# Kernel optimization log

Measured on AMD Instinct MI355X. Metric: run time of the kernel, lower is better.

## Reference

```python
import jax, jax.numpy as jnp
import numpy as np

H, NH, NKV, HD, FF = 2048, 16, 8, 128, 6144
S, T = 2048, 4096
EPS, THETA, NEG = 1e-6, 1e6, -1e9

def _rms(x, w, eps=EPS):
    return x * jax.lax.rsqrt(jnp.mean(x * x, axis=-1, keepdims=True) + eps) * w

def _rotate_half(x):
    d = x.shape[-1] // 2
    return jnp.concatenate([-x[..., d:], x[..., :d]], axis=-1)

def _rope(positions, hd, theta=THETA):
    inv_freq = 1.0 / (theta ** (jnp.arange(0, hd, 2, dtype=jnp.float32) / hd))
    freqs = positions.astype(jnp.float32)[..., None] * inv_freq  # [B,S,hd/2]
    emb = jnp.concatenate([freqs, freqs], axis=-1)               # [B,S,hd]
    return jnp.cos(emb), jnp.sin(emb)

def setup_inputs() -> dict:
    key = jax.random.key(0)
    ks = jax.random.split(key, 12)
    hidden_states = jax.random.normal(ks[0], (1, S, H), jnp.float32) * 0.02
    i = jnp.arange(T)
    causal_mask = jnp.where(i[None, :] <= i[:, None], 0.0, NEG).astype(jnp.float32)[None, None]
    idxs = jnp.sort(jax.random.randint(ks[1], (S,), 0, T - 1, jnp.int32)).at[-1].set(T - 1)
    w = lambda k, sh: jax.random.normal(k, sh, jnp.float32) * 0.02
    return dict(
        hidden_states=hidden_states, causal_mask=causal_mask,
        keys_idxs=idxs, hs_idxs=idxs, positions=idxs[None, :],
        ln_in_w=jnp.ones((H,), jnp.float32),
        q_w=w(ks[2], (H, NH * HD)), k_w=w(ks[3], (H, NKV * HD)), v_w=w(ks[4], (H, NKV * HD)),
        q_norm_w=jnp.ones((HD,), jnp.float32), k_norm_w=jnp.ones((HD,), jnp.float32),
        o_w=w(ks[5], (NH * HD, H)), ln_post_w=jnp.ones((H,), jnp.float32),
        gate_w=w(ks[6], (H, FF)), up_w=w(ks[7], (H, FF)), down_w=w(ks[8], (FF, H)),
    )

def reference(hidden_states, causal_mask, keys_idxs, hs_idxs, positions,
              ln_in_w, q_w, k_w, v_w, q_norm_w, k_norm_w, o_w,
              ln_post_w, gate_w, up_w, down_w):
    B, Sq, _ = hidden_states.shape
    hd = q_norm_w.shape[0]
    nh = q_w.shape[1] // hd
    nkv = k_w.shape[1] // hd
    scaling = hd ** -0.5

    # gather pruned causal mask: index_select dim 3 (keys), then dim 2 (queries)
    mask = causal_mask[:, :, :, keys_idxs][:, :, hs_idxs, :]  # [B,1,Sq,Sk]

    cos, sin = _rope(positions, hd)  # [B,Sq,hd]

    x = _rms(hidden_states, ln_in_w)
    q = _rms((x @ q_w).reshape(B, Sq, nh, hd), q_norm_w).swapaxes(1, 2)   # [B,nh,Sq,hd]
    k = _rms((x @ k_w).reshape(B, Sq, nkv, hd), k_norm_w).swapaxes(1, 2)  # [B,nkv,Sq,hd]
    v = (x @ v_w).reshape(B, Sq, nkv, hd).swapaxes(1, 2)

    c, s = cos[:, None], sin[:, None]
    q = q * c + _rotate_half(q) * s
    k = k * c + _rotate_half(k) * s

    groups = nh // nkv
    k_rep = jnp.repeat(k, groups, axis=1)
    v_rep = jnp.repeat(v, groups, axis=1)

    # token-importance from last query (last original token kept at slot Sq-1)
    q_last = q[:, :, -1:, :]
    imp = jax.nn.softmax(jnp.einsum('bhqd,bhkd->bhqk', q_last, k_rep) * scaling, axis=-1)
    importance = imp[0, :, 0, :].mean(axis=0)
    importance = jax.lax.stop_gradient(importance.at[Sq - 1].set(jnp.inf))

    scores = jnp.einsum('bhqd,bhkd->bhqk', q, k_rep) * scaling + mask
    attn = jax.nn.softmax(scores, axis=-1)
    ctx = jnp.einsum('bhqk,bhkd->bhqd', attn, v_rep)
    attn_out = ctx.swapaxes(1, 2).reshape(B, Sq, nh * hd) @ o_w

    h = hidden_states + attn_out
    y = _rms(h, ln_post_w)
    mlp = (jax.nn.silu(y @ gate_w) * (y @ up_w)) @ down_w
    out = h + mlp
    return out, importance
```

## Files before the change

kernel.cpp:

```cpp
#include <hip/hip_runtime.h>
#include <math.h>

#define S_LEN 2048
#define HDIM  2048
#define NHEADS 16
#define NKVH   8
#define HD     128
#define FFDIM  6144
#define EPSV   1e-6f

__device__ __forceinline__ ushort f2bf(float f) {
    unsigned u = __float_as_uint(f);
    u += 0x7FFF + ((u >> 16) & 1);
    return (ushort)(u >> 16);
}
__device__ __forceinline__ float bf2f(ushort h) {
    return __uint_as_float(((unsigned)h) << 16);
}

typedef __attribute__((ext_vector_type(8))) short bf16x8;
typedef __attribute__((ext_vector_type(4))) float f32x4;

__device__ __forceinline__ void glds16(const void* g, void* l) {
    __builtin_amdgcn_global_load_lds(
        (const __attribute__((address_space(1))) void*)g,
        (__attribute__((address_space(3))) void*)l, 16, 0, 0);
}

__global__ __launch_bounds__(256) void rmsnorm_split_k(const float* __restrict__ in,
                                                       const float* __restrict__ w,
                                                       ushort* __restrict__ oh,
                                                       ushort* __restrict__ ol) {
    int s = blockIdx.x;
    int tid = threadIdx.x;
    const float* row = in + (size_t)s * HDIM;
    float ss = 0.0f;
    for (int i = tid; i < HDIM; i += 256) {
        float v = row[i];
        ss += v * v;
    }
    __shared__ float red[256];
    red[tid] = ss;
    __syncthreads();
    for (int off = 128; off > 0; off >>= 1) {
        if (tid < off) red[tid] += red[tid + off];
        __syncthreads();
    }
    float r = rsqrtf(red[0] / (float)HDIM + EPSV);
    for (int i = tid; i < HDIM; i += 256) {
        float v = row[i] * r * w[i];
        ushort h = f2bf(v);
        oh[(size_t)s * HDIM + i] = h;
        ol[(size_t)s * HDIM + i] = f2bf(v - bf2f(h));
    }
}

__global__ __launch_bounds__(256) void split_k(const float* __restrict__ in,
                                               ushort* __restrict__ oh,
                                               ushort* __restrict__ ol, int n) {
    int i = blockIdx.x * 256 + threadIdx.x;
    if (i < n) {
        float v = in[i];
        ushort h = f2bf(v);
        oh[i] = h;
        ol[i] = f2bf(v - bf2f(h));
    }
}

__global__ __launch_bounds__(256) void conv_k_swz_k(const float* __restrict__ in,
                                                    ushort* __restrict__ oh,
                                                    ushort* __restrict__ ol) {
    int i = blockIdx.x * 256 + threadIdx.x;
    int s = i >> 10;
    int d = i & 127;
    int base = i & ~127;
    float v = in[i];
    unsigned u = __float_as_uint(v);
    float hi = __uint_as_float(u & 0xFFFF0000u);
    int o = base + (d ^ ((s & 7) << 3));
    oh[o] = (ushort)(u >> 16);
    ol[o] = (ushort)(__float_as_uint(v - hi) >> 16);
}

__global__ __launch_bounds__(256) void conv_vt_k(const float* __restrict__ v,
                                                 ushort* __restrict__ oh,
                                                 ushort* __restrict__ ol) {
    __shared__ float t[64][65];
    int s0 = blockIdx.x * 64, d0 = blockIdx.y * 64, kvh = blockIdx.z;
    int tid = threadIdx.x;
#pragma unroll
    for (int p = 0; p < 4; ++p) {
        int c = tid + p * 256;
        int ss = c >> 4, d4 = (c & 15) * 4;
        float4 x = *(const float4*)&v[((size_t)(s0 + ss) * NKVH + kvh) * HD + d0 + d4];
        t[d4 + 0][ss] = x.x;
        t[d4 + 1][ss] = x.y;
        t[d4 + 2][ss] = x.z;
        t[d4 + 3][ss] = x.w;
    }
    __syncthreads();
#pragma unroll
    for (int p = 0; p < 4; ++p) {
        int c = tid + p * 256;
        int dd = c >> 4, s4 = (c & 15) * 4;
        int d = d0 + dd;
        int sx = s4 ^ ((d & 7) << 3);
        size_t obase = ((size_t)kvh * HD + d) * S_LEN + s0 + sx;
        ushort4 hv, lv;
        float a0 = t[dd][s4 + 0], a1 = t[dd][s4 + 1], a2 = t[dd][s4 + 2], a3 = t[dd][s4 + 3];
        unsigned u0 = __float_as_uint(a0), u1 = __float_as_uint(a1);
        unsigned u2 = __float_as_uint(a2), u3 = __float_as_uint(a3);
        hv.x = (ushort)(u0 >> 16); lv.x = (ushort)(__float_as_uint(a0 - __uint_as_float(u0 & 0xFFFF0000u)) >> 16);
        hv.y = (ushort)(u1 >> 16); lv.y = (ushort)(__float_as_uint(a1 - __uint_as_float(u1 & 0xFFFF0000u)) >> 16);
        hv.z = (ushort)(u2 >> 16); lv.z = (ushort)(__float_as_uint(a2 - __uint_as_float(u2 & 0xFFFF0000u)) >> 16);
        hv.w = (ushort)(u3 >> 16); lv.w = (ushort)(__float_as_uint(a3 - __uint_as_float(u3 & 0xFFFF0000u)) >> 16);
        *(ushort4*)&oh[obase] = hv;
        *(ushort4*)&ol[obase] = lv;
    }
}

__global__ __launch_bounds__(256) void transpose_split_k(const float* __restrict__ W,
                                                         ushort* __restrict__ Th,
                                                         ushort* __restrict__ Tl,
                                                         int K, int Ntot, int n0) {
    __shared__ float t[64][65];
    int tid = threadIdx.x;
    int nt = blockIdx.x * 64;
    int kt = blockIdx.y * 64;
#pragma unroll
    for (int p = 0; p < 4; ++p) {
        int idx = tid + p * 256;
        int kk = idx >> 4;
        int nn = (idx & 15) * 4;
        float4 v = *(const float4*)&W[(size_t)(kt + kk) * Ntot + n0 + nt + nn];
        t[nn + 0][kk] = v.x;
        t[nn + 1][kk] = v.y;
        t[nn + 2][kk] = v.z;
        t[nn + 3][kk] = v.w;
    }
    __syncthreads();
#pragma unroll
    for (int p = 0; p < 4; ++p) {
        int idx = tid + p * 256;
        int nn = idx >> 4;
        int kk = (idx & 15) * 4;
        ushort4 hv, lv;
        float a0 = t[nn][kk + 0], a1 = t[nn][kk + 1], a2 = t[nn][kk + 2], a3 = t[nn][kk + 3];
        hv.x = f2bf(a0); lv.x = f2bf(a0 - bf2f(hv.x));
        hv.y = f2bf(a1); lv.y = f2bf(a1 - bf2f(hv.y));
        hv.z = f2bf(a2); lv.z = f2bf(a2 - bf2f(hv.z));
        hv.w = f2bf(a3); lv.w = f2bf(a3 - bf2f(hv.w));
        size_t o = (size_t)(nt + nn) * K + kt + kk;
        *(ushort4*)&Th[o] = hv;
        *(ushort4*)&Tl[o] = lv;
    }
}

template <int MODE>
__global__ __launch_bounds__(256, 3) void gemm_bf16x3(
    const ushort* __restrict__ Ah, const ushort* __restrict__ Al,
    const ushort* __restrict__ Bh, const ushort* __restrict__ Bl,
    const float* res, const float* __restrict__ gbuf,
    float* C, ushort* __restrict__ Dh, ushort* __restrict__ Dl,
    int M, int N, int K) {
    __shared__ __align__(16) ushort sA[2 * 64 * 32];
    __shared__ __align__(16) ushort sB[2 * 128 * 32];

    unsigned nbx = gridDim.x;
    unsigned flat = blockIdx.y * nbx + blockIdx.x;
    unsigned cpx = (nbx * gridDim.y) >> 3;
    unsigned sflat = (flat & 7u) * cpx + (flat >> 3);
    int bx = (int)(sflat % nbx);
    int by = (int)(sflat / nbx);
    int bm = by * 64, bn = bx * 128;

    int tid = threadIdx.x;
    int lane = tid & 63, wave = tid >> 6;

    int srow = tid >> 2;
    int sk = (tid & 3) * 8;
    const ushort* gAh = Ah + (size_t)(bm + srow) * K + sk;
    const ushort* gAl = Al + (size_t)(bm + srow) * K + sk;
    const ushort* gB0h = Bh + (size_t)(bn + srow) * K + sk;
    const ushort* gB0l = Bl + (size_t)(bn + srow) * K + sk;
    const ushort* gB1h = Bh + (size_t)(bn + 64 + srow) * K + sk;
    const ushort* gB1l = Bl + (size_t)(bn + 64 + srow) * K + sk;
    ushort* lAh = sA + tid * 8;
    ushort* lAl = sA + 2048 + tid * 8;
    ushort* lB0h = sB + tid * 8;
    ushort* lB1h = sB + 2048 + tid * 8;
    ushort* lB0l = sB + 4096 + tid * 8;
    ushort* lB1l = sB + 6144 + tid * 8;

    int r = lane & 15, kq = lane >> 4;
    const ushort* pA = sA + r * 32 + kq * 8;
    const ushort* pB = sB + (wave * 32 + r) * 32 + kq * 8;

    f32x4 acc[4][2] = {};

    for (int k0 = 0; k0 < K; k0 += 32) {
        glds16(gAh, lAh);
        glds16(gAl, lAl);
        glds16(gB0h, lB0h);
        glds16(gB1h, lB1h);
        glds16(gB0l, lB0l);
        glds16(gB1l, lB1l);
        gAh += 32; gAl += 32; gB0h += 32; gB0l += 32; gB1h += 32; gB1l += 32;
        __syncthreads();

        bf16x8 ah[4], al[4], bh[2], bl[2];
#pragma unroll
        for (int mi = 0; mi < 4; ++mi) {
            ah[mi] = *(const bf16x8*)(pA + mi * 512);
            al[mi] = *(const bf16x8*)(pA + 2048 + mi * 512);
        }
#pragma unroll
        for (int ni = 0; ni < 2; ++ni) {
            bh[ni] = *(const bf16x8*)(pB + ni * 512);
            bl[ni] = *(const bf16x8*)(pB + 4096 + ni * 512);
        }
#pragma unroll
        for (int mi = 0; mi < 4; ++mi)
#pragma unroll
            for (int ni = 0; ni < 2; ++ni) {
                acc[mi][ni] = __builtin_amdgcn_mfma_f32_16x16x32_bf16(ah[mi], bh[ni], acc[mi][ni], 0, 0, 0);
                acc[mi][ni] = __builtin_amdgcn_mfma_f32_16x16x32_bf16(al[mi], bh[ni], acc[mi][ni], 0, 0, 0);
                acc[mi][ni] = __builtin_amdgcn_mfma_f32_16x16x32_bf16(ah[mi], bl[ni], acc[mi][ni], 0, 0, 0);
            }
        __syncthreads();
    }

    int c0 = bn + wave * 32 + (lane & 15);
    int r0 = bm + (lane >> 4) * 4;
#pragma unroll
    for (int mi = 0; mi < 4; ++mi)
#pragma unroll
        for (int ni = 0; ni < 2; ++ni)
#pragma unroll
            for (int j = 0; j < 4; ++j) {
                int row = r0 + mi * 16 + j;
                int col = c0 + ni * 16;
                size_t idx = (size_t)row * N + col;
                float val = acc[mi][ni][j];
                if (MODE == 0) {
                    if (res) val += res[idx];
                    C[idx] = val;
                } else {
                    float gv = gbuf[idx];
                    float dv = gv / (1.0f + expf(-gv)) * val;
                    ushort hh = f2bf(dv);
                    Dh[idx] = hh;
                    Dl[idx] = f2bf(dv - bf2f(hh));
                }
            }
}

__global__ __launch_bounds__(128) void qk_norm_rope_k(float* __restrict__ qk,
                                                      const float* __restrict__ nw,
                                                      const int* __restrict__ positions,
                                                      int nheads) {
    int s = blockIdx.x;
    int h = blockIdx.y;
    int d = threadIdx.x;
    float* row = qk + ((size_t)s * nheads + h) * HD;
    __shared__ float buf[HD];
    __shared__ float red[HD];
    float v = row[d];
    red[d] = v * v;
    __syncthreads();
    for (int off = 64; off > 0; off >>= 1) {
        if (d < off) red[d] += red[d + off];
        __syncthreads();
    }
    float r = rsqrtf(red[0] / (float)HD + EPSV);
    float nv = v * r * nw[d];
    buf[d] = nv;
    __syncthreads();
    float pos = (float)positions[s];
    int d2 = d & 63;
    float inv_freq = expf(-((float)(2 * d2) / 128.0f) * 13.815510557964274f);
    float freq = pos * inv_freq;
    float c, sn;
    sincosf(freq, &sn, &c);
    float rot = (d < 64) ? -buf[d + 64] : buf[d - 64];
    row[d] = nv * c + rot * sn;
}

#define ATQ 64
#define ATK 64

__global__ __launch_bounds__(256, 2) void attn_mfma_k(
    const ushort* __restrict__ Qhg, const ushort* __restrict__ Qlg,
    const ushort* __restrict__ Khg, const ushort* __restrict__ Klg,
    const ushort* __restrict__ Vhg, const ushort* __restrict__ Vlg,
    const int* __restrict__ keys_idxs, const int* __restrict__ hs_idxs,
    float* __restrict__ ctx) {
    __shared__ __align__(16) ushort sKh[64 * 128];
    __shared__ __align__(16) ushort sKl[64 * 128];
    __shared__ __align__(16) ushort sVh[128 * 64];
    __shared__ __align__(16) ushort sVl[128 * 64];
    __shared__ int kidx[ATK];
    __shared__ int qpos[ATQ];

    int bx = blockIdx.x;
    int qt = (bx & 1) ? (31 - (bx >> 1)) : (bx >> 1);
    int h = blockIdx.y;
    int kvh = h >> 1;
    int tid = threadIdx.x;
    int lane = tid & 63, wv = tid >> 6;
    int q0 = qt * ATQ;
    int r = lane & 15, kq = lane >> 4;
    int xorv = (lane & 7) << 3;
    const float scale = 0.088388347648318447f;

    bf16x8 qh[4], ql[4];
    {
        const ushort* qb = Qhg + ((size_t)(q0 + wv * 16 + r) * NHEADS + h) * HD + kq * 8;
        const ushort* qb2 = Qlg + ((size_t)(q0 + wv * 16 + r) * NHEADS + h) * HD + kq * 8;
#pragma unroll
        for (int ks = 0; ks < 4; ++ks) {
            qh[ks] = *(const bf16x8*)(qb + ks * 32);
            ql[ks] = *(const bf16x8*)(qb2 + ks * 32);
        }
    }
    if (tid < ATQ) qpos[tid] = hs_idxs[q0 + tid];

    const size_t kvstride = (size_t)NKVH * HD;
    const ushort* gKh = Khg + ((size_t)(tid >> 4) * NKVH + kvh) * HD + (tid & 15) * 8;
    const ushort* gKl = Klg + ((size_t)(tid >> 4) * NKVH + kvh) * HD + (tid & 15) * 8;
    const ushort* gVh = Vhg + ((size_t)kvh * HD + (tid >> 3)) * S_LEN + (tid & 7) * 8;
    const ushort* gVl = Vlg + ((size_t)kvh * HD + (tid >> 3)) * S_LEN + (tid & 7) * 8;

    f32x4 o[8] = {};
    float m_run[4] = {-3.0e38f, -3.0e38f, -3.0e38f, -3.0e38f};
    float l_run[4] = {0.0f, 0.0f, 0.0f, 0.0f};

    __syncthreads();
    int hs_max = qpos[ATQ - 1];
    int qp[4];
#pragma unroll
    for (int j = 0; j < 4; ++j) qp[j] = qpos[wv * 16 + kq * 4 + j];

    for (int kt = 0; kt < S_LEN / ATK; ++kt) {
        int k0 = kt * ATK;
        if (keys_idxs[k0] > hs_max) break;
        __syncthreads();
        const size_t koff = (size_t)k0 * kvstride;
#pragma unroll
        for (int p = 0; p < 4; ++p) {
            glds16(gKh + koff + (size_t)p * 16 * kvstride, sKh + (tid + p * 256) * 8);
            glds16(gKl + koff + (size_t)p * 16 * kvstride, sKl + (tid + p * 256) * 8);
            glds16(gVh + k0 + (size_t)p * 32 * S_LEN, sVh + (tid + p * 256) * 8);
            glds16(gVl + k0 + (size_t)p * 32 * S_LEN, sVl + (tid + p * 256) * 8);
        }
        if (tid < ATK) kidx[tid] = keys_idxs[k0 + tid];
        __syncthreads();

        f32x4 sf[4] = {};
#pragma unroll
        for (int ks = 0; ks < 4; ++ks) {
            int kb = (ks * 32 + kq * 8) ^ xorv;
#pragma unroll
            for (int f = 0; f < 4; ++f) {
                bf16x8 kh = *(const bf16x8*)(sKh + (f * 16 + r) * 128 + kb);
                bf16x8 kl = *(const bf16x8*)(sKl + (f * 16 + r) * 128 + kb);
                sf[f] = __builtin_amdgcn_mfma_f32_16x16x32_bf16(qh[ks], kh, sf[f], 0, 0, 0);
                sf[f] = __builtin_amdgcn_mfma_f32_16x16x32_bf16(ql[ks], kh, sf[f], 0, 0, 0);
                sf[f] = __builtin_amdgcn_mfma_f32_16x16x32_bf16(qh[ks], kl, sf[f], 0, 0, 0);
            }
        }

        int kj[4];
#pragma unroll
        for (int f = 0; f < 4; ++f) kj[f] = kidx[f * 16 + r];
        float alj[4];
#pragma unroll
        for (int j = 0; j < 4; ++j) {
#pragma unroll
            for (int f = 0; f < 4; ++f)
                sf[f][j] = sf[f][j] * scale + ((kj[f] <= qp[j]) ? 0.0f : -1.0e9f);
            float m0 = fmaxf(fmaxf(sf[0][j], sf[1][j]), fmaxf(sf[2][j], sf[3][j]));
#pragma unroll
            for (int off = 1; off < 16; off <<= 1) m0 = fmaxf(m0, __shfl_xor(m0, off));
            float mn = fmaxf(m_run[j], m0);
            alj[j] = __expf(m_run[j] - mn);
            m_run[j] = mn;
            float rsum = 0.0f;
#pragma unroll
            for (int f = 0; f < 4; ++f) {
                sf[f][j] = __expf(sf[f][j] - mn);
                rsum += sf[f][j];
            }
#pragma unroll
            for (int off = 1; off < 16; off <<= 1) rsum += __shfl_xor(rsum, off);
            l_run[j] = l_run[j] * alj[j] + rsum;
        }
#pragma unroll
        for (int df = 0; df < 8; ++df)
#pragma unroll
            for (int j = 0; j < 4; ++j) o[df][j] *= alj[j];

        __syncthreads();

        ushort* sPh = sKh + wv * 2048;
        ushort* sPl = sPh + 1024;
#pragma unroll
        for (int j = 0; j < 4; ++j) {
            int qloc = kq * 4 + j;
            int swz = (qloc & 7) << 3;
            int rowb = qloc * 64;
#pragma unroll
            for (int f = 0; f < 4; ++f) {
                float pv = sf[f][j];
                unsigned u = __float_as_uint(pv);
                float hi = __uint_as_float(u & 0xFFFF0000u);
                int a = rowb + ((f * 16 + r) ^ swz);
                sPh[a] = (ushort)(u >> 16);
                sPl[a] = (ushort)(__float_as_uint(pv - hi) >> 16);
            }
        }

#pragma unroll
        for (int kv0 = 0; kv0 < 2; ++kv0) {
            int kb = (kv0 * 32 + kq * 8) ^ xorv;
            bf16x8 pah = *(const bf16x8*)(sPh + r * 64 + kb);
            bf16x8 pal = *(const bf16x8*)(sPl + r * 64 + kb);
#pragma unroll
            for (int df = 0; df < 8; ++df) {
                bf16x8 vh = *(const bf16x8*)(sVh + (df * 16 + r) * 64 + kb);
                bf16x8 vl = *(const bf16x8*)(sVl + (df * 16 + r) * 64 + kb);
                o[df] = __builtin_amdgcn_mfma_f32_16x16x32_bf16(pah, vh, o[df], 0, 0, 0);
                o[df] = __builtin_amdgcn_mfma_f32_16x16x32_bf16(pal, vh, o[df], 0, 0, 0);
                o[df] = __builtin_amdgcn_mfma_f32_16x16x32_bf16(pah, vl, o[df], 0, 0, 0);
            }
        }
    }

#pragma unroll
    for (int j = 0; j < 4; ++j) {
        float invl = 1.0f / l_run[j];
        int qg = q0 + wv * 16 + kq * 4 + j;
#pragma unroll
        for (int df = 0; df < 8; ++df) {
            int d = df * 16 + r;
            ctx[((size_t)qg * NHEADS + h) * HD + d] = o[df][j] * invl;
        }
    }
}

__global__ __launch_bounds__(256) void importance_scores_k(const float* __restrict__ q,
                                                           const float* __restrict__ k,
                                                           float* __restrict__ imp_ws) {
    int h = blockIdx.x;
    int kv = h >> 1;
    int tid = threadIdx.x;
    __shared__ float qrow[HD];
    __shared__ float sc[S_LEN];
    __shared__ float red[256];
    const float* qp = q + ((size_t)(S_LEN - 1) * NHEADS + h) * HD;
    if (tid < HD) qrow[tid] = qp[tid];
    __syncthreads();
    const float scale = 0.088388347648318447f;
    float lmax = -3.0e38f;
#pragma unroll
    for (int rep = 0; rep < 8; ++rep) {
        int j = tid + rep * 256;
        const float* kp = k + ((size_t)j * NKVH + kv) * HD;
        float dot = 0.0f;
        for (int d = 0; d < HD; ++d) dot += qrow[d] * kp[d];
        float sval = dot * scale;
        sc[j] = sval;
        lmax = fmaxf(lmax, sval);
    }
    red[tid] = lmax;
    __syncthreads();
    for (int off = 128; off > 0; off >>= 1) {
        if (tid < off) red[tid] = fmaxf(red[tid], red[tid + off]);
        __syncthreads();
    }
    float m = red[0];
    __syncthreads();
    float lsum = 0.0f;
    float evals[8];
#pragma unroll
    for (int rep = 0; rep < 8; ++rep) {
        int j = tid + rep * 256;
        float e = expf(sc[j] - m);
        evals[rep] = e;
        lsum += e;
    }
    red[tid] = lsum;
    __syncthreads();
    for (int off = 128; off > 0; off >>= 1) {
        if (tid < off) red[tid] += red[tid + off];
        __syncthreads();
    }
    float inv = 1.0f / red[0];
#pragma unroll
    for (int rep = 0; rep < 8; ++rep) {
        int j = tid + rep * 256;
        imp_ws[(size_t)h * S_LEN + j] = evals[rep] * inv;
    }
}

__global__ __launch_bounds__(256) void importance_combine_k(const float* __restrict__ imp_ws,
                                                            float* __restrict__ out) {
    int j = blockIdx.x * 256 + threadIdx.x;
    float sum = 0.0f;
    for (int h = 0; h < NHEADS; ++h) sum += imp_ws[(size_t)h * S_LEN + j];
    out[j] = (j == S_LEN - 1) ? 3.0e38f : sum * (1.0f / NHEADS);
}

extern "C" void kernel_launch(void* const* d_in, const int* in_sizes, int n_in,
                              void* d_out, int out_size, void* d_ws, size_t ws_size,
                              hipStream_t stream) {
    const float* hidden    = (const float*)d_in[0];
    const int*   keys_idxs = (const int*)d_in[2];
    const int*   hs_idxs   = (const int*)d_in[3];
    const int*   positions = (const int*)d_in[4];
    const float* ln_in_w   = (const float*)d_in[5];
    const float* q_w       = (const float*)d_in[6];
    const float* k_w       = (const float*)d_in[7];
    const float* v_w       = (const float*)d_in[8];
    const float* q_norm_w  = (const float*)d_in[9];
    const float* k_norm_w  = (const float*)d_in[10];
    const float* o_w       = (const float*)d_in[11];
    const float* ln_post_w = (const float*)d_in[12];
    const float* gate_w    = (const float*)d_in[13];
    const float* up_w      = (const float*)d_in[14];
    const float* down_w    = (const float*)d_in[15];

    float* out = (float*)d_out;
    float* ws = (float*)d_ws;
    const size_t MF = 1024ull * 1024;

    ushort* Xh = (ushort*)(ws);
    ushort* Xl = (ushort*)(ws + 2 * MF);
    ushort* Wh = (ushort*)(ws + 4 * MF);
    ushort* Wl = (ushort*)(ws + 6 * MF);
    float*  qb  = ws + 8 * MF;
    float*  kbf = ws + 12 * MF;
    float*  vbf = ws + 14 * MF;
    float*  ctx = ws + 16 * MF;
    ushort* Qbh = (ushort*)(ws);
    ushort* Qbl = (ushort*)(ws + 2 * MF);
    float*  imp = ws + 4 * MF;
    ushort* Kbh = (ushort*)(ws + 4 * MF);
    ushort* Kbl = (ushort*)(ws + 5 * MF);
    ushort* Vth = (ushort*)(ws + 6 * MF);
    ushort* Vtl = (ushort*)(ws + 7 * MF);
    ushort* Ch = (ushort*)(ws + 8 * MF);
    ushort* Cl = (ushort*)(ws + 10 * MF);
    float*  hb = ws + 12 * MF;
    ushort* Yh = (ushort*)(ws + 16 * MF);
    ushort* Yl = (ushort*)(ws + 18 * MF);
    float*  gb = ws + 8 * MF;
    ushort* Dh = (ushort*)(ws + 12 * MF);
    ushort* Dl = (ushort*)(ws + 14 * MF);

    rmsnorm_split_k<<<S_LEN, 256, 0, stream>>>(hidden, ln_in_w, Xh, Xl);

    transpose_split_k<<<dim3(32, 32), 256, 0, stream>>>(q_w, Wh, Wl, HDIM, HDIM, 0);
    gemm_bf16x3<0><<<dim3(HDIM / 128, S_LEN / 64), 256, 0, stream>>>(
        Xh, Xl, Wh, Wl, nullptr, nullptr, qb, nullptr, nullptr, S_LEN, HDIM, HDIM);

    transpose_split_k<<<dim3(16, 32), 256, 0, stream>>>(k_w, Wh, Wl, HDIM, 1024, 0);
    gemm_bf16x3<0><<<dim3(1024 / 128, S_LEN / 64), 256, 0, stream>>>(
        Xh, Xl, Wh, Wl, nullptr, nullptr, kbf, nullptr, nullptr, S_LEN, 1024, HDIM);

    transpose_split_k<<<dim3(16, 32), 256, 0, stream>>>(v_w, Wh, Wl, HDIM, 1024, 0);
    gemm_bf16x3<0><<<dim3(1024 / 128, S_LEN / 64), 256, 0, stream>>>(
        Xh, Xl, Wh, Wl, nullptr, nullptr, vbf, nullptr, nullptr, S_LEN, 1024, HDIM);

    qk_norm_rope_k<<<dim3(S_LEN, NHEADS), 128, 0, stream>>>(qb, q_norm_w, positions, NHEADS);
    qk_norm_rope_k<<<dim3(S_LEN, NKVH), 128, 0, stream>>>(kbf, k_norm_w, positions, NKVH);

    importance_scores_k<<<NHEADS, 256, 0, stream>>>(qb, kbf, imp);
    importance_combine_k<<<S_LEN / 256, 256, 0, stream>>>(imp, out + (size_t)S_LEN * HDIM);

    split_k<<<(S_LEN * NHEADS * HD) / 256, 256, 0, stream>>>(qb, Qbh, Qbl, S_LEN * NHEADS * HD);
    conv_k_swz_k<<<(S_LEN * NKVH * HD) / 256, 256, 0, stream>>>(kbf, Kbh, Kbl);
    conv_vt_k<<<dim3(S_LEN / 64, HD / 64, NKVH), 256, 0, stream>>>(vbf, Vth, Vtl);

    attn_mfma_k<<<dim3(S_LEN / ATQ, NHEADS), 256, 0, stream>>>(
        Qbh, Qbl, Kbh, Kbl, Vth, Vtl, keys_idxs, hs_idxs, ctx);

    split_k<<<(S_LEN * HDIM) / 256, 256, 0, stream>>>(ctx, Ch, Cl, S_LEN * HDIM);
    transpose_split_k<<<dim3(32, 32), 256, 0, stream>>>(o_w, Wh, Wl, HDIM, HDIM, 0);
    gemm_bf16x3<0><<<dim3(HDIM / 128, S_LEN / 64), 256, 0, stream>>>(
        Ch, Cl, Wh, Wl, hidden, nullptr, hb, S_LEN ? nullptr : nullptr, nullptr, S_LEN, HDIM, HDIM);

    hipMemcpyAsync(out, hb, (size_t)S_LEN * HDIM * sizeof(float),
                   hipMemcpyDeviceToDevice, stream);

    rmsnorm_split_k<<<S_LEN, 256, 0, stream>>>(hb, ln_post_w, Yh, Yl);

    for (int c = 0; c < 3; ++c) {
        transpose_split_k<<<dim3(32, 32), 256, 0, stream>>>(gate_w, Wh, Wl, HDIM, FFDIM, c * 2048);
        gemm_bf16x3<0><<<dim3(16, 32), 256, 0, stream>>>(
            Yh, Yl, Wh, Wl, nullptr, nullptr, gb, nullptr, nullptr, S_LEN, 2048, HDIM);
        transpose_split_k<<<dim3(32, 32), 256, 0, stream>>>(up_w, Wh, Wl, HDIM, FFDIM, c * 2048);
        gemm_bf16x3<1><<<dim3(16, 32), 256, 0, stream>>>(
            Yh, Yl, Wh, Wl, nullptr, gb, nullptr, Dh, Dl, S_LEN, 2048, HDIM);
        transpose_split_k<<<dim3(32, 32), 256, 0, stream>>>(
            down_w + (size_t)c * 2048 * HDIM, Wh, Wl, 2048, HDIM, 0);
        gemm_bf16x3<0><<<dim3(16, 32), 256, 0, stream>>>(
            Dh, Dl, Wh, Wl, out, nullptr, out, nullptr, nullptr, S_LEN, HDIM, 2048);
    }
}
```

Before: 1.427 ms.

## Enlarge GEMM tile to 128x128 with 2x2 waves; fuse ctx split into attention

The bf16x3 GEMM block tile grows from 64x128 to 128x128, with waves arranged 2x2 so each wave computes a 64x64 sub-tile using 16 accumulators. This raises operand reuse per LDS load and halves global traffic per output, but doubles the register footprint and cuts grid size, so occupancy may drop with launch bounds of 3 blocks per SM. The attention kernel now writes the hi/lo bf16 split of the context directly, which removes the fp32 ctx buffer and the separate split kernel pass.

```diff
diff --git a/kernel.cpp b/kernel.cpp
--- a/kernel.cpp
+++ b/kernel.cpp
@@ -163,8 +163,10 @@
     const float* res, const float* __restrict__ gbuf,
     float* C, ushort* __restrict__ Dh, ushort* __restrict__ Dl,
     int M, int N, int K) {
-    __shared__ __align__(16) ushort sA[2 * 64 * 32];
-    __shared__ __align__(16) ushort sB[2 * 128 * 32];
+    __shared__ __align__(16) ushort sAh[128 * 32];
+    __shared__ __align__(16) ushort sAl[128 * 32];
+    __shared__ __align__(16) ushort sBh[128 * 32];
+    __shared__ __align__(16) ushort sBl[128 * 32];
 
     unsigned nbx = gridDim.x;
     unsigned flat = blockIdx.y * nbx + blockIdx.x;
@@ -172,70 +174,66 @@
     unsigned sflat = (flat & 7u) * cpx + (flat >> 3);
     int bx = (int)(sflat % nbx);
     int by = (int)(sflat / nbx);
-    int bm = by * 64, bn = bx * 128;
+    int bm = by * 128, bn = bx * 128;
 
     int tid = threadIdx.x;
     int lane = tid & 63, wave = tid >> 6;
+    int wr = wave >> 1, wc = wave & 1;
+    int r = lane & 15, kq = lane >> 4;
 
     int srow = tid >> 2;
     int sk = (tid & 3) * 8;
-    const ushort* gAh = Ah + (size_t)(bm + srow) * K + sk;
-    const ushort* gAl = Al + (size_t)(bm + srow) * K + sk;
+    const ushort* gA0h = Ah + (size_t)(bm + srow) * K + sk;
+    const ushort* gA0l = Al + (size_t)(bm + srow) * K + sk;
     const ushort* gB0h = Bh + (size_t)(bn + srow) * K + sk;
     const ushort* gB0l = Bl + (size_t)(bn + srow) * K + sk;
-    const ushort* gB1h = Bh + (size_t)(bn + 64 + srow) * K + sk;
-    const ushort* gB1l = Bl + (size_t)(bn + 64 + srow) * K + sk;
-    ushort* lAh = sA + tid * 8;
-    ushort* lAl = sA + 2048 + tid * 8;
-    ushort* lB0h = sB + tid * 8;
-    ushort* lB1h = sB + 2048 + tid * 8;
-    ushort* lB0l = sB + 4096 + tid * 8;
-    ushort* lB1l = sB + 6144 + tid * 8;
-
-    int r = lane & 15, kq = lane >> 4;
-    const ushort* pA = sA + r * 32 + kq * 8;
-    const ushort* pB = sB + (wave * 32 + r) * 32 + kq * 8;
-
-    f32x4 acc[4][2] = {};
+    const size_t rstep = (size_t)64 * K;
+
+    const ushort* pAh = sAh + (wr * 64 + r) * 32 + kq * 8;
+    const ushort* pAl = sAl + (wr * 64 + r) * 32 + kq * 8;
+    const ushort* pBh = sBh + (wc * 64 + r) * 32 + kq * 8;
+    const ushort* pBl = sBl + (wc * 64 + r) * 32 + kq * 8;
+
+    f32x4 acc[4][4] = {};
 
     for (int k0 = 0; k0 < K; k0 += 32) {
-        glds16(gAh, lAh);
-        glds16(gAl, lAl);
-        glds16(gB0h, lB0h);
-        glds16(gB1h, lB1h);
-        glds16(gB0l, lB0l);
-        glds16(gB1l, lB1l);
-        gAh += 32; gAl += 32; gB0h += 32; gB0l += 32; gB1h += 32; gB1l += 32;
-        __syncthreads();
-
-        bf16x8 ah[4], al[4], bh[2], bl[2];
+        glds16(gA0h, sAh + tid * 8);
+        glds16(gA0h + rstep, sAh + 2048 + tid * 8);
+        glds16(gA0l, sAl + tid * 8);
+        glds16(gA0l + rstep, sAl + 2048 + tid * 8);
+        glds16(gB0h, sBh + tid * 8);
+        glds16(gB0h + rstep, sBh + 2048 + tid * 8);
+        glds16(gB0l, sBl + tid * 8);
+        glds16(gB0l + rstep, sBl + 2048 + tid * 8);
+        gA0h += 32; gA0l += 32; gB0h += 32; gB0l += 32;
+        __syncthreads();
+
+        bf16x8 ah[4], al[4];
 #pragma unroll
         for (int mi = 0; mi < 4; ++mi) {
-            ah[mi] = *(const bf16x8*)(pA + mi * 512);
-            al[mi] = *(const bf16x8*)(pA + 2048 + mi * 512);
-        }
-#pragma unroll
-        for (int ni = 0; ni < 2; ++ni) {
-            bh[ni] = *(const bf16x8*)(pB + ni * 512);
-            bl[ni] = *(const bf16x8*)(pB + 4096 + ni * 512);
-        }
-#pragma unroll
-        for (int mi = 0; mi < 4; ++mi)
-#pragma unroll
-            for (int ni = 0; ni < 2; ++ni) {
-                acc[mi][ni] = __builtin_amdgcn_mfma_f32_16x16x32_bf16(ah[mi], bh[ni], acc[mi][ni], 0, 0, 0);
-                acc[mi][ni] = __builtin_amdgcn_mfma_f32_16x16x32_bf16(al[mi], bh[ni], acc[mi][ni], 0, 0, 0);
-                acc[mi][ni] = __builtin_amdgcn_mfma_f32_16x16x32_bf16(ah[mi], bl[ni], acc[mi][ni], 0, 0, 0);
+            ah[mi] = *(const bf16x8*)(pAh + mi * 512);
+            al[mi] = *(const bf16x8*)(pAl + mi * 512);
+        }
+#pragma unroll
+        for (int ni = 0; ni < 4; ++ni) {
+            bf16x8 bh = *(const bf16x8*)(pBh + ni * 512);
+            bf16x8 bl = *(const bf16x8*)(pBl + ni * 512);
+#pragma unroll
+            for (int mi = 0; mi < 4; ++mi) {
+                acc[mi][ni] = __builtin_amdgcn_mfma_f32_16x16x32_bf16(ah[mi], bh, acc[mi][ni], 0, 0, 0);
+                acc[mi][ni] = __builtin_amdgcn_mfma_f32_16x16x32_bf16(al[mi], bh, acc[mi][ni], 0, 0, 0);
+                acc[mi][ni] = __builtin_amdgcn_mfma_f32_16x16x32_bf16(ah[mi], bl, acc[mi][ni], 0, 0, 0);
             }
-        __syncthreads();
-    }
-
-    int c0 = bn + wave * 32 + (lane & 15);
-    int r0 = bm + (lane >> 4) * 4;
+        }
+        __syncthreads();
+    }
+
+    int c0 = bn + wc * 64 + r;
+    int r0 = bm + wr * 64 + kq * 4;
 #pragma unroll
     for (int mi = 0; mi < 4; ++mi)
 #pragma unroll
-        for (int ni = 0; ni < 2; ++ni)
+        for (int ni = 0; ni < 4; ++ni)
 #pragma unroll
             for (int j = 0; j < 4; ++j) {
                 int row = r0 + mi * 16 + j;
@@ -294,7 +292,7 @@
     const ushort* __restrict__ Khg, const ushort* __restrict__ Klg,
     const ushort* __restrict__ Vhg, const ushort* __restrict__ Vlg,
     const int* __restrict__ keys_idxs, const int* __restrict__ hs_idxs,
-    float* __restrict__ ctx) {
+    ushort* __restrict__ Chg, ushort* __restrict__ Clg) {
     __shared__ __align__(16) ushort sKh[64 * 128];
     __shared__ __align__(16) ushort sKl[64 * 128];
     __shared__ __align__(16) ushort sVh[128 * 64];
@@ -443,7 +441,11 @@
 #pragma unroll
         for (int df = 0; df < 8; ++df) {
             int d = df * 16 + r;
-            ctx[((size_t)qg * NHEADS + h) * HD + d] = o[df][j] * invl;
+            float val = o[df][j] * invl;
+            size_t idx = ((size_t)qg * NHEADS + h) * HD + d;
+            ushort hh = f2bf(val);
+            Chg[idx] = hh;
+            Clg[idx] = f2bf(val - bf2f(hh));
         }
     }
 }
@@ -541,7 +543,6 @@
     float*  qb  = ws + 8 * MF;
     float*  kbf = ws + 12 * MF;
     float*  vbf = ws + 14 * MF;
-    float*  ctx = ws + 16 * MF;
     ushort* Qbh = (ushort*)(ws);
     ushort* Qbl = (ushort*)(ws + 2 * MF);
     float*  imp = ws + 4 * MF;
@@ -561,15 +562,15 @@
     rmsnorm_split_k<<<S_LEN, 256, 0, stream>>>(hidden, ln_in_w, Xh, Xl);
 
     transpose_split_k<<<dim3(32, 32), 256, 0, stream>>>(q_w, Wh, Wl, HDIM, HDIM, 0);
-    gemm_bf16x3<0><<<dim3(HDIM / 128, S_LEN / 64), 256, 0, stream>>>(
+    gemm_bf16x3<0><<<dim3(HDIM / 128, S_LEN / 128), 256, 0, stream>>>(
         Xh, Xl, Wh, Wl, nullptr, nullptr, qb, nullptr, nullptr, S_LEN, HDIM, HDIM);
 
     transpose_split_k<<<dim3(16, 32), 256, 0, stream>>>(k_w, Wh, Wl, HDIM, 1024, 0);
-    gemm_bf16x3<0><<<dim3(1024 / 128, S_LEN / 64), 256, 0, stream>>>(
+    gemm_bf16x3<0><<<dim3(1024 / 128, S_LEN / 128), 256, 0, stream>>>(
         Xh, Xl, Wh, Wl, nullptr, nullptr, kbf, nullptr, nullptr, S_LEN, 1024, HDIM);
 
     transpose_split_k<<<dim3(16, 32), 256, 0, stream>>>(v_w, Wh, Wl, HDIM, 1024, 0);
-    gemm_bf16x3<0><<<dim3(1024 / 128, S_LEN / 64), 256, 0, stream>>>(
+    gemm_bf16x3<0><<<dim3(1024 / 128, S_LEN / 128), 256, 0, stream>>>(
         Xh, Xl, Wh, Wl, nullptr, nullptr, vbf, nullptr, nullptr, S_LEN, 1024, HDIM);
 
     qk_norm_rope_k<<<dim3(S_LEN, NHEADS), 128, 0, stream>>>(qb, q_norm_w, positions, NHEADS);
@@ -583,12 +584,11 @@
     conv_vt_k<<<dim3(S_LEN / 64, HD / 64, NKVH), 256, 0, stream>>>(vbf, Vth, Vtl);
 
     attn_mfma_k<<<dim3(S_LEN / ATQ, NHEADS), 256, 0, stream>>>(
-        Qbh, Qbl, Kbh, Kbl, Vth, Vtl, keys_idxs, hs_idxs, ctx);
-
-    split_k<<<(S_LEN * HDIM) / 256, 256, 0, stream>>>(ctx, Ch, Cl, S_LEN * HDIM);
+        Qbh, Qbl, Kbh, Kbl, Vth, Vtl, keys_idxs, hs_idxs, Ch, Cl);
+
     transpose_split_k<<<dim3(32, 32), 256, 0, stream>>>(o_w, Wh, Wl, HDIM, HDIM, 0);
-    gemm_bf16x3<0><<<dim3(HDIM / 128, S_LEN / 64), 256, 0, stream>>>(
-        Ch, Cl, Wh, Wl, hidden, nullptr, hb, S_LEN ? nullptr : nullptr, nullptr, S_LEN, HDIM, HDIM);
+    gemm_bf16x3<0><<<dim3(HDIM / 128, S_LEN / 128), 256, 0, stream>>>(
+        Ch, Cl, Wh, Wl, hidden, nullptr, hb, nullptr, nullptr, S_LEN, HDIM, HDIM);
 
     hipMemcpyAsync(out, hb, (size_t)S_LEN * HDIM * sizeof(float),
                    hipMemcpyDeviceToDevice, stream);
@@ -597,14 +597,14 @@
 
     for (int c = 0; c < 3; ++c) {
         transpose_split_k<<<dim3(32, 32), 256, 0, stream>>>(gate_w, Wh, Wl, HDIM, FFDIM, c * 2048);
-        gemm_bf16x3<0><<<dim3(16, 32), 256, 0, stream>>>(
+        gemm_bf16x3<0><<<dim3(16, 16), 256, 0, stream>>>(
             Yh, Yl, Wh, Wl, nullptr, nullptr, gb, nullptr, nullptr, S_LEN, 2048, HDIM);
         transpose_split_k<<<dim3(32, 32), 256, 0, stream>>>(up_w, Wh, Wl, HDIM, FFDIM, c * 2048);
-        gemm_bf16x3<1><<<dim3(16, 32), 256, 0, stream>>>(
+        gemm_bf16x3<1><<<dim3(16, 16), 256, 0, stream>>>(
             Yh, Yl, Wh, Wl, nullptr, gb, nullptr, Dh, Dl, S_LEN, 2048, HDIM);
         transpose_split_k<<<dim3(32, 32), 256, 0, stream>>>(
             down_w + (size_t)c * 2048 * HDIM, Wh, Wl, 2048, HDIM, 0);
-        gemm_bf16x3<0><<<dim3(16, 32), 256, 0, stream>>>(
+        gemm_bf16x3<0><<<dim3(16, 16), 256, 0, stream>>>(
             Dh, Dl, Wh, Wl, out, nullptr, out, nullptr, nullptr, S_LEN, HDIM, 2048);
     }
 }
```

After: 1.687 ms. 18.2% more time.
